# Kernel tuning notes

Hardware: AMD Instinct MI355X
Metric: run time of the kernel (lower is better)

The kernel has to match this reference:

```python
import jax, jax.numpy as jnp
import numpy as np

N = 50000
E = 1_600_000


def spmm(edge_index, edge_weight, support, num_nodes):
    # adj[i, j] = w for (i=row, j=col); out[i] = sum_j adj[i,j] * support[j]
    row, col = edge_index[0], edge_index[1]
    msgs = support[col] * edge_weight[:, None]  # [E, d] gather + scale
    return jax.ops.segment_sum(msgs, row, num_segments=num_nodes)


def setup_inputs() -> dict:
    key = jax.random.key(0)
    ks = jax.random.split(key, 7)
    x = jax.random.normal(ks[0], (N, 128), dtype=jnp.float32)
    edge_index = jax.random.randint(ks[1], (2, E), 0, N, dtype=jnp.int64)
    edge_weight = jax.random.uniform(ks[2], (E,), dtype=jnp.float32)
    W1 = jax.random.normal(ks[3], (128, 128), dtype=jnp.float32) * (1.0 / np.sqrt(128))
    b1 = jax.random.normal(ks[4], (128,), dtype=jnp.float32) * (1.0 / np.sqrt(128))
    W2 = jax.random.normal(ks[5], (128, 40), dtype=jnp.float32) * (1.0 / np.sqrt(40))
    b2 = jax.random.normal(ks[6], (40,), dtype=jnp.float32) * (1.0 / np.sqrt(40))
    return {"x": x, "edge_index": edge_index, "edge_weight": edge_weight,
            "W1": W1, "b1": b1, "W2": W2, "b2": b2}


def reference(x, edge_index, edge_weight, W1, b1, W2, b2):
    n = x.shape[0]
    # layer 1: GraphConvolution + ReLU (dropout p=0.0 -> no-op)
    h = spmm(edge_index, edge_weight, x @ W1, n) + b1
    h = jax.nn.relu(h)
    # layer 2: GraphConvolution
    out = spmm(edge_index, edge_weight, h @ W2, n) + b2
    return jax.nn.log_softmax(out, axis=1)
```

## Files before the change

### kernel.cpp

```cpp
#include <hip/hip_runtime.h>
#include <hip/hip_fp16.h>
#include <math.h>

#define N_NODES 50000
#define N_EDGES 1600000
#define D1 128
#define D2 40
#define D2P 64
#define BROWS 128
#define NB 391
#define CHUNK 6250
#define CSR_CAP 7000

typedef __attribute__((ext_vector_type(8))) short bf16x8;
typedef __attribute__((ext_vector_type(4))) float f32x4;

__device__ __forceinline__ void bf16_split(float v, unsigned short& h, unsigned short& l) {
    unsigned u = __float_as_uint(v);
    unsigned r = u + 0x7fffu + ((u >> 16) & 1u);
    h = (unsigned short)(r >> 16);
    float hf = __uint_as_float((unsigned)h << 16);
    float lof = v - hf;
    unsigned u2 = __float_as_uint(lof);
    unsigned r2 = u2 + 0x7fffu + ((u2 >> 16) & 1u);
    l = (unsigned short)(r2 >> 16);
}

__device__ __forceinline__ int detect_is64_block(const unsigned int* ei) {
    __shared__ int any;
    if (threadIdx.x == 0) any = 0;
    __syncthreads();
    int a = 0;
    for (int i = threadIdx.x; i < 2048; i += 256) a |= (ei[2 * i + 1] != 0u);
    if (a) any = 1;
    __syncthreads();
    return any ? 0 : 1;
}

__device__ __forceinline__ int edge_row(const unsigned int* ei, int e, int is64) {
    return (int)(is64 ? ei[2 * e] : ei[e]);
}
__device__ __forceinline__ int edge_col(const unsigned int* ei, int e, int is64) {
    return (int)(is64 ? ei[2 * (N_EDGES + e)] : ei[N_EDGES + e]);
}

__global__ __launch_bounds__(256) void prep_k(const float* __restrict__ W1,
                                              unsigned short* __restrict__ wh1,
                                              unsigned short* __restrict__ wl1,
                                              const float* __restrict__ W2,
                                              unsigned short* __restrict__ wh2,
                                              unsigned short* __restrict__ wl2) {
    int b = blockIdx.x, t = threadIdx.x;
    if (b < 64) {
        int idx = b * 256 + t;
        int k = idx >> 7, n = idx & 127;
        unsigned short h, l;
        bf16_split(W1[k * 128 + n], h, l);
        int nt = n >> 4, ks = k >> 5;
        int lane = (n & 15) | (((k >> 3) & 3) << 4);
        int j = k & 7;
        int dst = ((nt * 4 + ks) * 64 + lane) * 8 + j;
        wh1[dst] = h;
        wl1[dst] = l;
    } else {
        int idx = (b - 64) * 256 + t;
        int k = idx >> 6, n = idx & 63;
        float v = (n < D2) ? W2[k * D2 + n] : 0.f;
        unsigned short h, l;
        bf16_split(v, h, l);
        int nt = n >> 4, ks = k >> 5;
        int lane = (n & 15) | (((k >> 3) & 3) << 4);
        int j = k & 7;
        int dst = ((nt * 4 + ks) * 64 + lane) * 8 + j;
        wh2[dst] = h;
        wl2[dst] = l;
    }
}

__global__ __launch_bounds__(256) void bin_k(const unsigned int* __restrict__ ei,
                                             const float* __restrict__ ew,
                                             unsigned int* __restrict__ gbhp,
                                             uint2* __restrict__ tmp8,
                                             unsigned int* __restrict__ bofs) {
    __shared__ uint2 lrec[CHUNK];
    __shared__ unsigned int lh[NB];
    __shared__ unsigned int lstart[NB + 1];
    __shared__ unsigned int lcur[NB];
    __shared__ unsigned int ssum[256];
    int b = blockIdx.x, t = threadIdx.x;
    int is64 = detect_is64_block(ei);
    for (int i = t; i < NB; i += 256) lh[i] = 0;
    __syncthreads();
    int e0 = b * CHUNK, e1 = e0 + CHUNK;
    for (int e = e0 + t; e < e1; e += 256) {
        atomicAdd(&lh[edge_row(ei, e, is64) >> 7], 1u);
    }
    __syncthreads();
    for (int i = t; i < NB; i += 256) {
        if (lh[i]) atomicAdd(&gbhp[i * 16], lh[i]);
    }
    unsigned int lsum = 0;
    if (t < 196) {
        lsum = lh[2 * t];
        if (2 * t + 1 < NB) lsum += lh[2 * t + 1];
    }
    ssum[t] = lsum;
    __syncthreads();
    for (int off = 1; off < 256; off <<= 1) {
        unsigned int add = (t >= off) ? ssum[t - off] : 0u;
        __syncthreads();
        ssum[t] += add;
        __syncthreads();
    }
    unsigned int run = (t == 0) ? 0u : ssum[t - 1];
    if (t < 196) {
        lstart[2 * t] = run;
        if (2 * t + 1 < NB) lstart[2 * t + 1] = run + lh[2 * t];
    }
    if (t == 0) lstart[NB] = CHUNK;
    __syncthreads();
    for (int i = t; i < NB; i += 256) lcur[i] = lstart[i];
    __syncthreads();
    for (int e = e0 + t; e < e1; e += 256) {
        int r = edge_row(ei, e, is64);
        int c = edge_col(ei, e, is64);
        unsigned int p = atomicAdd(&lcur[r >> 7], 1u);
        uint2 rec;
        rec.x = ((unsigned int)r << 16) | (unsigned int)c;
        rec.y = __float_as_uint(ew[e]);
        lrec[p] = rec;
    }
    __syncthreads();
    for (int i = t; i <= NB; i += 256) bofs[b * (NB + 1) + i] = lstart[i];
    for (int p = t; p < CHUNK; p += 256) tmp8[e0 + p] = lrec[p];
}

__global__ __launch_bounds__(512) void bscan_k(const unsigned int* __restrict__ gbhp,
                                               int* __restrict__ bbase) {
    __shared__ unsigned int s[512];
    int t = threadIdx.x;
    unsigned int v = (t < NB) ? gbhp[t * 16] : 0u;
    s[t] = v;
    __syncthreads();
    for (int off = 1; off < 512; off <<= 1) {
        unsigned int add = (t >= off) ? s[t - off] : 0u;
        __syncthreads();
        s[t] += add;
        __syncthreads();
    }
    if (t < NB) bbase[t] = (int)(s[t] - v);
    if (t == NB - 1) bbase[NB] = (int)s[t];
}

__global__ __launch_bounds__(256) void csr_k(const uint2* __restrict__ tmp8,
                                             const unsigned int* __restrict__ bofs,
                                             const int* __restrict__ bbase,
                                             int* __restrict__ rowptr,
                                             uint2* __restrict__ colwS) {
    __shared__ uint2 lrec[CSR_CAP];
    __shared__ unsigned int ssum[256];
    __shared__ unsigned int rcnt[BROWS];
    __shared__ unsigned int loff[BROWS];
    __shared__ unsigned int lcur[BROWS];
    int b = blockIdx.x, t = threadIdx.x;
    unsigned int mystart = bofs[t * (NB + 1) + b];
    unsigned int myend = bofs[t * (NB + 1) + b + 1];
    unsigned int mycnt = myend - mystart;
    ssum[t] = mycnt;
    __syncthreads();
    for (int off = 1; off < 256; off <<= 1) {
        unsigned int add = (t >= off) ? ssum[t - off] : 0u;
        __syncthreads();
        ssum[t] += add;
        __syncthreads();
    }
    unsigned int mybase = ssum[t] - mycnt;
    unsigned int total = ssum[255];
    const uint2* src = &tmp8[t * CHUNK + mystart];
    for (unsigned int k = 0; k < mycnt; ++k) lrec[mybase + k] = src[k];
    if (t < BROWS) rcnt[t] = 0;
    __syncthreads();
    for (unsigned int p = t; p < total; p += 256) {
        atomicAdd(&rcnt[(lrec[p].x >> 16) & 127], 1u);
    }
    __syncthreads();
    if (t < BROWS) loff[t] = rcnt[t];
    __syncthreads();
    for (int off = 1; off < BROWS; off <<= 1) {
        unsigned int add = (t >= off && t < BROWS) ? loff[t - off] : 0u;
        __syncthreads();
        if (t < BROWS) loff[t] += add;
        __syncthreads();
    }
    int lo = bbase[b], hi = bbase[b + 1];
    int r0 = b * BROWS;
    int nrows = N_NODES - r0;
    if (nrows > BROWS) nrows = BROWS;
    if (t < BROWS) {
        unsigned int excl = loff[t] - rcnt[t];
        if (t < nrows) rowptr[r0 + t] = lo + (int)excl;
        lcur[t] = (unsigned int)lo + excl;
    }
    if (b == NB - 1 && t == 0) rowptr[N_NODES] = hi;
    __syncthreads();
    for (unsigned int p = t; p < total; p += 256) {
        uint2 rec = lrec[p];
        unsigned int rl = (rec.x >> 16) & 127;
        unsigned int pos = atomicAdd(&lcur[rl], 1u);
        uint2 cw;
        cw.x = rec.x & 0xFFFFu;
        cw.y = rec.y;
        colwS[pos] = cw;
    }
}

__global__ __launch_bounds__(256) void gemm1_k(const float* __restrict__ x,
                                               const unsigned short* __restrict__ wh,
                                               const unsigned short* __restrict__ wl,
                                               __half* __restrict__ Ah) {
    int t = threadIdx.x;
    int w = t >> 6, l = t & 63;
    int row0 = blockIdx.x * 64 + w * 16;
    int arow = row0 + (l & 15);
    if (arow > N_NODES - 1) arow = N_NODES - 1;
    int kbase = (l >> 4) * 8;
    bf16x8 ah[4], al[4];
#pragma unroll
    for (int ks = 0; ks < 4; ++ks) {
        const float* px = &x[arow * D1 + ks * 32 + kbase];
        float4 v0 = *reinterpret_cast<const float4*>(px);
        float4 v1 = *reinterpret_cast<const float4*>(px + 4);
        float vv[8] = {v0.x, v0.y, v0.z, v0.w, v1.x, v1.y, v1.z, v1.w};
#pragma unroll
        for (int j = 0; j < 8; ++j) {
            unsigned short h, lo2;
            bf16_split(vv[j], h, lo2);
            ah[ks][j] = (short)h;
            al[ks][j] = (short)lo2;
        }
    }
    f32x4 acc[8];
#pragma unroll
    for (int nt = 0; nt < 8; ++nt) acc[nt] = (f32x4)(0.f);
#pragma unroll
    for (int nt = 0; nt < 8; ++nt) {
#pragma unroll
        for (int ks = 0; ks < 4; ++ks) {
            int fo = ((nt * 4 + ks) * 64 + l) * 8;
            bf16x8 bh = *reinterpret_cast<const bf16x8*>(&wh[fo]);
            bf16x8 bl = *reinterpret_cast<const bf16x8*>(&wl[fo]);
            acc[nt] = __builtin_amdgcn_mfma_f32_16x16x32_bf16(ah[ks], bh, acc[nt], 0, 0, 0);
            acc[nt] = __builtin_amdgcn_mfma_f32_16x16x32_bf16(ah[ks], bl, acc[nt], 0, 0, 0);
            acc[nt] = __builtin_amdgcn_mfma_f32_16x16x32_bf16(al[ks], bh, acc[nt], 0, 0, 0);
        }
    }
    int crow0 = row0 + (l >> 4) * 4;
    int ccol = l & 15;
#pragma unroll
    for (int nt = 0; nt < 8; ++nt) {
#pragma unroll
        for (int r = 0; r < 4; ++r) {
            int rr = crow0 + r;
            if (rr < N_NODES) Ah[rr * D1 + nt * 16 + ccol] = __float2half_rn(acc[nt][r]);
        }
    }
}

__global__ __launch_bounds__(256) void spmm1_k(const __half* __restrict__ Ah,
                                               const int* __restrict__ rowptr,
                                               const uint2* __restrict__ colwS,
                                               __half* __restrict__ Bh) {
    int t = threadIdx.x;
    int r = blockIdx.x * 4 + (t >> 6);
    int lane = t & 63;
    int half = lane >> 5;
    int cg = lane & 31;
    int s = rowptr[r], e = rowptr[r + 1];
    float4 acc = {0.f, 0.f, 0.f, 0.f};
#pragma unroll 4
    for (int j = s + half; j < e; j += 2) {
        uint2 cw = colwS[j];
        float w = __uint_as_float(cw.y);
        uint2 q = *reinterpret_cast<const uint2*>(&Ah[cw.x * D1 + cg * 4]);
        float2 f0 = __half22float2(*reinterpret_cast<const __half2*>(&q.x));
        float2 f1 = __half22float2(*reinterpret_cast<const __half2*>(&q.y));
        acc.x += w * f0.x;
        acc.y += w * f0.y;
        acc.z += w * f1.x;
        acc.w += w * f1.y;
    }
    acc.x += __shfl_xor(acc.x, 32);
    acc.y += __shfl_xor(acc.y, 32);
    acc.z += __shfl_xor(acc.z, 32);
    acc.w += __shfl_xor(acc.w, 32);
    if (half == 0) {
        unsigned p0 = ((unsigned)__half_as_ushort(__float2half_rn(acc.y)) << 16) |
                      __half_as_ushort(__float2half_rn(acc.x));
        unsigned p1 = ((unsigned)__half_as_ushort(__float2half_rn(acc.w)) << 16) |
                      __half_as_ushort(__float2half_rn(acc.z));
        uint2 st;
        st.x = p0;
        st.y = p1;
        *reinterpret_cast<uint2*>(&Bh[r * D1 + cg * 4]) = st;
    }
}

__global__ __launch_bounds__(256) void gemm2_k(const __half* __restrict__ Bh,
                                               const float* __restrict__ b1,
                                               const unsigned short* __restrict__ wh,
                                               const unsigned short* __restrict__ wl,
                                               __half* __restrict__ Gh) {
    int t = threadIdx.x;
    int w = t >> 6, l = t & 63;
    int row0 = blockIdx.x * 64 + w * 16;
    int arow = row0 + (l & 15);
    if (arow > N_NODES - 1) arow = N_NODES - 1;
    int kbase = (l >> 4) * 8;
    bf16x8 ah[4], al[4];
#pragma unroll
    for (int ks = 0; ks < 4; ++ks) {
        const __half* pb = &Bh[arow * D1 + ks * 32 + kbase];
        const float* pb1 = &b1[ks * 32 + kbase];
        uint4 q = *reinterpret_cast<const uint4*>(pb);
        float2 g0 = __half22float2(*reinterpret_cast<const __half2*>(&q.x));
        float2 g1 = __half22float2(*reinterpret_cast<const __half2*>(&q.y));
        float2 g2 = __half22float2(*reinterpret_cast<const __half2*>(&q.z));
        float2 g3 = __half22float2(*reinterpret_cast<const __half2*>(&q.w));
        float4 c0 = *reinterpret_cast<const float4*>(pb1);
        float4 c1 = *reinterpret_cast<const float4*>(pb1 + 4);
        float vv[8] = {g0.x + c0.x, g0.y + c0.y, g1.x + c0.z, g1.y + c0.w,
                       g2.x + c1.x, g2.y + c1.y, g3.x + c1.z, g3.y + c1.w};
#pragma unroll
        for (int j = 0; j < 8; ++j) {
            float rv = vv[j] > 0.f ? vv[j] : 0.f;
            unsigned short h, lo2;
            bf16_split(rv, h, lo2);
            ah[ks][j] = (short)h;
            al[ks][j] = (short)lo2;
        }
    }
    f32x4 acc[4];
#pragma unroll
    for (int nt = 0; nt < 4; ++nt) acc[nt] = (f32x4)(0.f);
#pragma unroll
    for (int nt = 0; nt < 4; ++nt) {
#pragma unroll
        for (int ks = 0; ks < 4; ++ks) {
            int fo = ((nt * 4 + ks) * 64 + l) * 8;
            bf16x8 bh = *reinterpret_cast<const bf16x8*>(&wh[fo]);
            bf16x8 bl = *reinterpret_cast<const bf16x8*>(&wl[fo]);
            acc[nt] = __builtin_amdgcn_mfma_f32_16x16x32_bf16(ah[ks], bh, acc[nt], 0, 0, 0);
            acc[nt] = __builtin_amdgcn_mfma_f32_16x16x32_bf16(ah[ks], bl, acc[nt], 0, 0, 0);
            acc[nt] = __builtin_amdgcn_mfma_f32_16x16x32_bf16(al[ks], bh, acc[nt], 0, 0, 0);
        }
    }
    int crow0 = row0 + (l >> 4) * 4;
    int ccol = l & 15;
#pragma unroll
    for (int nt = 0; nt < 4; ++nt) {
        int col = nt * 16 + ccol;
#pragma unroll
        for (int r = 0; r < 4; ++r) {
            int rr = crow0 + r;
            if (rr < N_NODES) Gh[rr * D2P + col] = __float2half_rn(acc[nt][r]);
        }
    }
}

__global__ __launch_bounds__(256) void spmm2lsm_k(const __half* __restrict__ Gh,
                                                  const int* __restrict__ rowptr,
                                                  const uint2* __restrict__ colwS,
                                                  const float* __restrict__ b2,
                                                  float* __restrict__ out) {
    int t = threadIdx.x;
    int r = blockIdx.x * 4 + (t >> 6);
    int lane = t & 63;
    int half = lane >> 5;
    int cg = lane & 31;
    int s = rowptr[r], e = rowptr[r + 1];
    float2 acc = {0.f, 0.f};
#pragma unroll 4
    for (int j = s + half; j < e; j += 2) {
        uint2 cw = colwS[j];
        float w = __uint_as_float(cw.y);
        unsigned q = *reinterpret_cast<const unsigned*>(&Gh[cw.x * D2P + cg * 2]);
        float2 f = __half22float2(*reinterpret_cast<const __half2*>(&q));
        acc.x += w * f.x;
        acc.y += w * f.y;
    }
    acc.x += __shfl_xor(acc.x, 32);
    acc.y += __shfl_xor(acc.y, 32);
    bool valid = lane < 20;
    float2 v2 = {-INFINITY, -INFINITY};
    if (valid) {
        float2 bv = reinterpret_cast<const float2*>(b2)[cg];
        v2.x = acc.x + bv.x;
        v2.y = acc.y + bv.y;
    }
    float m = fmaxf(v2.x, v2.y);
#pragma unroll
    for (int off = 1; off < 32; off <<= 1) m = fmaxf(m, __shfl_xor(m, off));
    float ex = valid ? expf(v2.x - m) + expf(v2.y - m) : 0.f;
#pragma unroll
    for (int off = 1; off < 32; off <<= 1) ex += __shfl_xor(ex, off);
    float lse = m + logf(ex);
    if (valid) {
        float2 o;
        o.x = v2.x - lse;
        o.y = v2.y - lse;
        *reinterpret_cast<float2*>(&out[r * D2 + cg * 2]) = o;
    }
}

extern "C" void kernel_launch(void* const* d_in, const int* in_sizes, int n_in,
                              void* d_out, int out_size, void* d_ws, size_t ws_size,
                              hipStream_t stream) {
    const float* x = (const float*)d_in[0];
    const unsigned int* ei = (const unsigned int*)d_in[1];
    const float* ew = (const float*)d_in[2];
    const float* W1 = (const float*)d_in[3];
    const float* b1 = (const float*)d_in[4];
    const float* W2 = (const float*)d_in[5];
    const float* b2 = (const float*)d_in[6];
    float* out = (float*)d_out;

    char* w = (char*)d_ws;
    __half* Ah = (__half*)w;
    __half* Bh = (__half*)(w + 12800000);
    uint2* tmp8 = (uint2*)(w + 25600000);
    __half* Gh = (__half*)(w + 38400000);
    uint2* colwS = (uint2*)(w + 44800000);
    int* rowptr = (int*)(w + 57600000);
    int* bbase = (int*)(w + 57800064);
    unsigned int* bofs = (unsigned int*)(w + 57801664);
    unsigned int* gbhp = (unsigned int*)(w + 58203072);
    unsigned short* wh1 = (unsigned short*)(w + 58228096);
    unsigned short* wl1 = (unsigned short*)(w + 58260864);
    unsigned short* wh2 = (unsigned short*)(w + 58293632);
    unsigned short* wl2 = (unsigned short*)(w + 58310016);

    hipMemsetAsync(gbhp, 0, NB * 64, stream);
    prep_k<<<96, 256, 0, stream>>>(W1, wh1, wl1, W2, wh2, wl2);
    bin_k<<<256, 256, 0, stream>>>(ei, ew, gbhp, tmp8, bofs);
    bscan_k<<<1, 512, 0, stream>>>(gbhp, bbase);
    gemm1_k<<<782, 256, 0, stream>>>(x, wh1, wl1, Ah);
    csr_k<<<NB, 256, 0, stream>>>(tmp8, bofs, bbase, rowptr, colwS);

    spmm1_k<<<N_NODES / 4, 256, 0, stream>>>(Ah, rowptr, colwS, Bh);
    gemm2_k<<<782, 256, 0, stream>>>(Bh, b1, wh2, wl2, Gh);
    spmm2lsm_k<<<N_NODES / 4, 256, 0, stream>>>(Gh, rowptr, colwS, b2, out);
}
```

Measured before the change: 260.0 us.

## Fuse layer-1 SpMM with bias/ReLU and second GEMM; fold scan and memset

Merges spmm1 and gemm2 into one kernel. Each block aggregates 16 rows into shared memory, applies bias and ReLU, then runs the split-bf16 MFMA against W2 directly, so the fp16 intermediate Bh is never written to or read back from global memory. The block-offset scan moves from its own single-block kernel into every csr_k block, which recomputes it redundantly. The gbhp memset moves into extra blocks of prep_k. Together these drop two kernel launches and one memset, at the cost of repeated scan work in csr_k and blocks of 16 rows with four waves each in the fused kernel.

```diff
diff --git a/kernel.cpp b/kernel.cpp
--- a/kernel.cpp
+++ b/kernel.cpp
@@ -49,7 +49,8 @@
                                               unsigned short* __restrict__ wl1,
                                               const float* __restrict__ W2,
                                               unsigned short* __restrict__ wh2,
-                                              unsigned short* __restrict__ wl2) {
+                                              unsigned short* __restrict__ wl2,
+                                              unsigned int* __restrict__ gbhp) {
     int b = blockIdx.x, t = threadIdx.x;
     if (b < 64) {
         int idx = b * 256 + t;
@@ -62,7 +63,7 @@
         int dst = ((nt * 4 + ks) * 64 + lane) * 8 + j;
         wh1[dst] = h;
         wl1[dst] = l;
-    } else {
+    } else if (b < 96) {
         int idx = (b - 64) * 256 + t;
         int k = idx >> 6, n = idx & 63;
         float v = (n < D2) ? W2[k * D2 + n] : 0.f;
@@ -74,6 +75,9 @@
         int dst = ((nt * 4 + ks) * 64 + lane) * 8 + j;
         wh2[dst] = h;
         wl2[dst] = l;
+    } else {
+        int idx = (b - 96) * 256 + t;
+        if (idx < NB * 16) gbhp[idx] = 0u;
     }
 }
 
@@ -135,34 +139,41 @@
     for (int p = t; p < CHUNK; p += 256) tmp8[e0 + p] = lrec[p];
 }
 
-__global__ __launch_bounds__(512) void bscan_k(const unsigned int* __restrict__ gbhp,
-                                               int* __restrict__ bbase) {
-    __shared__ unsigned int s[512];
-    int t = threadIdx.x;
-    unsigned int v = (t < NB) ? gbhp[t * 16] : 0u;
-    s[t] = v;
-    __syncthreads();
-    for (int off = 1; off < 512; off <<= 1) {
-        unsigned int add = (t >= off) ? s[t - off] : 0u;
-        __syncthreads();
-        s[t] += add;
-        __syncthreads();
-    }
-    if (t < NB) bbase[t] = (int)(s[t] - v);
-    if (t == NB - 1) bbase[NB] = (int)s[t];
-}
-
 __global__ __launch_bounds__(256) void csr_k(const uint2* __restrict__ tmp8,
                                              const unsigned int* __restrict__ bofs,
-                                             const int* __restrict__ bbase,
+                                             const unsigned int* __restrict__ gbhp,
                                              int* __restrict__ rowptr,
                                              uint2* __restrict__ colwS) {
     __shared__ uint2 lrec[CSR_CAP];
     __shared__ unsigned int ssum[256];
+    __shared__ unsigned int sv0[256];
     __shared__ unsigned int rcnt[BROWS];
     __shared__ unsigned int loff[BROWS];
     __shared__ unsigned int lcur[BROWS];
+    __shared__ int s_lo, s_hi;
     int b = blockIdx.x, t = threadIdx.x;
+    unsigned int v0 = (2 * t < NB) ? gbhp[(2 * t) * 16] : 0u;
+    unsigned int v1 = (2 * t + 1 < NB) ? gbhp[(2 * t + 1) * 16] : 0u;
+    sv0[t] = v0;
+    ssum[t] = v0 + v1;
+    __syncthreads();
+    for (int off = 1; off < 256; off <<= 1) {
+        unsigned int add = (t >= off) ? ssum[t - off] : 0u;
+        __syncthreads();
+        ssum[t] += add;
+        __syncthreads();
+    }
+    if (t == 0) {
+        int pi = b >> 1;
+        unsigned int lo = (pi == 0) ? 0u : ssum[pi - 1];
+        if (b & 1) lo += sv0[pi];
+        unsigned int cntb = (b & 1) ? (ssum[pi] - ((pi == 0) ? 0u : ssum[pi - 1]) - sv0[pi])
+                                    : sv0[pi];
+        s_lo = (int)lo;
+        s_hi = (int)(lo + cntb);
+    }
+    __syncthreads();
+    int lo = s_lo, hi = s_hi;
     unsigned int mystart = bofs[t * (NB + 1) + b];
     unsigned int myend = bofs[t * (NB + 1) + b + 1];
     unsigned int mycnt = myend - mystart;
@@ -192,7 +203,6 @@
         if (t < BROWS) loff[t] += add;
         __syncthreads();
     }
-    int lo = bbase[b], hi = bbase[b + 1];
     int r0 = b * BROWS;
     int nrows = N_NODES - r0;
     if (nrows > BROWS) nrows = BROWS;
@@ -266,104 +276,83 @@
     }
 }
 
-__global__ __launch_bounds__(256) void spmm1_k(const __half* __restrict__ Ah,
-                                               const int* __restrict__ rowptr,
-                                               const uint2* __restrict__ colwS,
-                                               __half* __restrict__ Bh) {
+__global__ __launch_bounds__(256) void spmm1g_k(const __half* __restrict__ Ah,
+                                                const int* __restrict__ rowptr,
+                                                const uint2* __restrict__ colwS,
+                                                const float* __restrict__ b1,
+                                                const unsigned short* __restrict__ wh,
+                                                const unsigned short* __restrict__ wl,
+                                                __half* __restrict__ Gh) {
+    __shared__ float hrow[16][132];
     int t = threadIdx.x;
-    int r = blockIdx.x * 4 + (t >> 6);
-    int lane = t & 63;
+    int w = t >> 6, lane = t & 63;
     int half = lane >> 5;
     int cg = lane & 31;
-    int s = rowptr[r], e = rowptr[r + 1];
-    float4 acc = {0.f, 0.f, 0.f, 0.f};
+    int row0 = blockIdx.x * 16;
+    float4 bv = *reinterpret_cast<const float4*>(&b1[cg * 4]);
+#pragma unroll
+    for (int i = 0; i < 4; ++i) {
+        int r = row0 + w * 4 + i;
+        int s = rowptr[r], e = rowptr[r + 1];
+        float4 acc = {0.f, 0.f, 0.f, 0.f};
 #pragma unroll 4
-    for (int j = s + half; j < e; j += 2) {
-        uint2 cw = colwS[j];
-        float w = __uint_as_float(cw.y);
-        uint2 q = *reinterpret_cast<const uint2*>(&Ah[cw.x * D1 + cg * 4]);
-        float2 f0 = __half22float2(*reinterpret_cast<const __half2*>(&q.x));
-        float2 f1 = __half22float2(*reinterpret_cast<const __half2*>(&q.y));
-        acc.x += w * f0.x;
-        acc.y += w * f0.y;
-        acc.z += w * f1.x;
-        acc.w += w * f1.y;
-    }
-    acc.x += __shfl_xor(acc.x, 32);
-    acc.y += __shfl_xor(acc.y, 32);
-    acc.z += __shfl_xor(acc.z, 32);
-    acc.w += __shfl_xor(acc.w, 32);
-    if (half == 0) {
-        unsigned p0 = ((unsigned)__half_as_ushort(__float2half_rn(acc.y)) << 16) |
-                      __half_as_ushort(__float2half_rn(acc.x));
-        unsigned p1 = ((unsigned)__half_as_ushort(__float2half_rn(acc.w)) << 16) |
-                      __half_as_ushort(__float2half_rn(acc.z));
-        uint2 st;
-        st.x = p0;
-        st.y = p1;
-        *reinterpret_cast<uint2*>(&Bh[r * D1 + cg * 4]) = st;
-    }
-}
-
-__global__ __launch_bounds__(256) void gemm2_k(const __half* __restrict__ Bh,
-                                               const float* __restrict__ b1,
-                                               const unsigned short* __restrict__ wh,
-                                               const unsigned short* __restrict__ wl,
-                                               __half* __restrict__ Gh) {
-    int t = threadIdx.x;
-    int w = t >> 6, l = t & 63;
-    int row0 = blockIdx.x * 64 + w * 16;
-    int arow = row0 + (l & 15);
-    if (arow > N_NODES - 1) arow = N_NODES - 1;
-    int kbase = (l >> 4) * 8;
+        for (int j = s + half; j < e; j += 2) {
+            uint2 cw = colwS[j];
+            float wv = __uint_as_float(cw.y);
+            uint2 q = *reinterpret_cast<const uint2*>(&Ah[cw.x * D1 + cg * 4]);
+            float2 f0 = __half22float2(*reinterpret_cast<const __half2*>(&q.x));
+            float2 f1 = __half22float2(*reinterpret_cast<const __half2*>(&q.y));
+            acc.x += wv * f0.x;
+            acc.y += wv * f0.y;
+            acc.z += wv * f1.x;
+            acc.w += wv * f1.y;
+        }
+        acc.x += __shfl_xor(acc.x, 32);
+        acc.y += __shfl_xor(acc.y, 32);
+        acc.z += __shfl_xor(acc.z, 32);
+        acc.w += __shfl_xor(acc.w, 32);
+        if (half == 0) {
+            float4 h;
+            h.x = fmaxf(acc.x + bv.x, 0.f);
+            h.y = fmaxf(acc.y + bv.y, 0.f);
+            h.z = fmaxf(acc.z + bv.z, 0.f);
+            h.w = fmaxf(acc.w + bv.w, 0.f);
+            *reinterpret_cast<float4*>(&hrow[w * 4 + i][cg * 4]) = h;
+        }
+    }
+    __syncthreads();
+    int l = lane;
+    int kb = (l >> 4) * 8;
     bf16x8 ah[4], al[4];
 #pragma unroll
     for (int ks = 0; ks < 4; ++ks) {
-        const __half* pb = &Bh[arow * D1 + ks * 32 + kbase];
-        const float* pb1 = &b1[ks * 32 + kbase];
-        uint4 q = *reinterpret_cast<const uint4*>(pb);
-        float2 g0 = __half22float2(*reinterpret_cast<const __half2*>(&q.x));
-        float2 g1 = __half22float2(*reinterpret_cast<const __half2*>(&q.y));
-        float2 g2 = __half22float2(*reinterpret_cast<const __half2*>(&q.z));
-        float2 g3 = __half22float2(*reinterpret_cast<const __half2*>(&q.w));
-        float4 c0 = *reinterpret_cast<const float4*>(pb1);
-        float4 c1 = *reinterpret_cast<const float4*>(pb1 + 4);
-        float vv[8] = {g0.x + c0.x, g0.y + c0.y, g1.x + c0.z, g1.y + c0.w,
-                       g2.x + c1.x, g2.y + c1.y, g3.x + c1.z, g3.y + c1.w};
+        const float* ph = &hrow[l & 15][ks * 32 + kb];
+        float4 v0 = *reinterpret_cast<const float4*>(ph);
+        float4 v1 = *reinterpret_cast<const float4*>(ph + 4);
+        float vv[8] = {v0.x, v0.y, v0.z, v0.w, v1.x, v1.y, v1.z, v1.w};
 #pragma unroll
         for (int j = 0; j < 8; ++j) {
-            float rv = vv[j] > 0.f ? vv[j] : 0.f;
             unsigned short h, lo2;
-            bf16_split(rv, h, lo2);
+            bf16_split(vv[j], h, lo2);
             ah[ks][j] = (short)h;
             al[ks][j] = (short)lo2;
         }
     }
-    f32x4 acc[4];
-#pragma unroll
-    for (int nt = 0; nt < 4; ++nt) acc[nt] = (f32x4)(0.f);
-#pragma unroll
-    for (int nt = 0; nt < 4; ++nt) {
-#pragma unroll
-        for (int ks = 0; ks < 4; ++ks) {
-            int fo = ((nt * 4 + ks) * 64 + l) * 8;
-            bf16x8 bh = *reinterpret_cast<const bf16x8*>(&wh[fo]);
-            bf16x8 bl = *reinterpret_cast<const bf16x8*>(&wl[fo]);
-            acc[nt] = __builtin_amdgcn_mfma_f32_16x16x32_bf16(ah[ks], bh, acc[nt], 0, 0, 0);
-            acc[nt] = __builtin_amdgcn_mfma_f32_16x16x32_bf16(ah[ks], bl, acc[nt], 0, 0, 0);
-            acc[nt] = __builtin_amdgcn_mfma_f32_16x16x32_bf16(al[ks], bh, acc[nt], 0, 0, 0);
-        }
+    f32x4 acc2 = (f32x4)(0.f);
+#pragma unroll
+    for (int ks = 0; ks < 4; ++ks) {
+        int fo = ((w * 4 + ks) * 64 + l) * 8;
+        bf16x8 bh = *reinterpret_cast<const bf16x8*>(&wh[fo]);
+        bf16x8 bl = *reinterpret_cast<const bf16x8*>(&wl[fo]);
+        acc2 = __builtin_amdgcn_mfma_f32_16x16x32_bf16(ah[ks], bh, acc2, 0, 0, 0);
+        acc2 = __builtin_amdgcn_mfma_f32_16x16x32_bf16(ah[ks], bl, acc2, 0, 0, 0);
+        acc2 = __builtin_amdgcn_mfma_f32_16x16x32_bf16(al[ks], bh, acc2, 0, 0, 0);
     }
     int crow0 = row0 + (l >> 4) * 4;
-    int ccol = l & 15;
-#pragma unroll
-    for (int nt = 0; nt < 4; ++nt) {
-        int col = nt * 16 + ccol;
-#pragma unroll
-        for (int r = 0; r < 4; ++r) {
-            int rr = crow0 + r;
-            if (rr < N_NODES) Gh[rr * D2P + col] = __float2half_rn(acc[nt][r]);
-        }
+    int ccol = w * 16 + (l & 15);
+#pragma unroll
+    for (int r = 0; r < 4; ++r) {
+        Gh[(crow0 + r) * D2P + ccol] = __float2half_rn(acc2[r]);
     }
 }
 
@@ -426,27 +415,22 @@
 
     char* w = (char*)d_ws;
     __half* Ah = (__half*)w;
-    __half* Bh = (__half*)(w + 12800000);
-    uint2* tmp8 = (uint2*)(w + 25600000);
-    __half* Gh = (__half*)(w + 38400000);
-    uint2* colwS = (uint2*)(w + 44800000);
-    int* rowptr = (int*)(w + 57600000);
-    int* bbase = (int*)(w + 57800064);
-    unsigned int* bofs = (unsigned int*)(w + 57801664);
-    unsigned int* gbhp = (unsigned int*)(w + 58203072);
-    unsigned short* wh1 = (unsigned short*)(w + 58228096);
-    unsigned short* wl1 = (unsigned short*)(w + 58260864);
-    unsigned short* wh2 = (unsigned short*)(w + 58293632);
-    unsigned short* wl2 = (unsigned short*)(w + 58310016);
-
-    hipMemsetAsync(gbhp, 0, NB * 64, stream);
-    prep_k<<<96, 256, 0, stream>>>(W1, wh1, wl1, W2, wh2, wl2);
+    uint2* tmp8 = (uint2*)(w + 12800000);
+    __half* Gh = (__half*)(w + 25600000);
+    uint2* colwS = (uint2*)(w + 32000000);
+    int* rowptr = (int*)(w + 44800000);
+    unsigned int* bofs = (unsigned int*)(w + 45000064);
+    unsigned int* gbhp = (unsigned int*)(w + 45401472);
+    unsigned short* wh1 = (unsigned short*)(w + 45426496);
+    unsigned short* wl1 = (unsigned short*)(w + 45459264);
+    unsigned short* wh2 = (unsigned short*)(w + 45492032);
+    unsigned short* wl2 = (unsigned short*)(w + 45508416);
+
+    prep_k<<<121, 256, 0, stream>>>(W1, wh1, wl1, W2, wh2, wl2, gbhp);
     bin_k<<<256, 256, 0, stream>>>(ei, ew, gbhp, tmp8, bofs);
-    bscan_k<<<1, 512, 0, stream>>>(gbhp, bbase);
     gemm1_k<<<782, 256, 0, stream>>>(x, wh1, wl1, Ah);
-    csr_k<<<NB, 256, 0, stream>>>(tmp8, bofs, bbase, rowptr, colwS);
-
-    spmm1_k<<<N_NODES / 4, 256, 0, stream>>>(Ah, rowptr, colwS, Bh);
-    gemm2_k<<<782, 256, 0, stream>>>(Bh, b1, wh2, wl2, Gh);
+    csr_k<<<NB, 256, 0, stream>>>(tmp8, bofs, gbhp, rowptr, colwS);
+
+    spmm1g_k<<<N_NODES / 16, 256, 0, stream>>>(Ah, rowptr, colwS, b1, wh2, wl2, Gh);
     spmm2lsm_k<<<N_NODES / 4, 256, 0, stream>>>(Gh, rowptr, colwS, b2, out);
 }
```

Result: faster. 253.8 us (-2.4%).
